# Optimization experiments

Measured on AMD Instinct MI355X. Metric: run time of the kernel, lower is better.

The kernel has to match this reference:

```python
import jax, jax.numpy as jnp
import numpy as np

BN_EPS = 1e-5
TN_EPS = 1e-4


def binarize(x):
    # Clipped straight-through binarization (Courbariaux BNN / Brevitas 1-bit):
    # forward = sign(x) in {-1,+1}, backward = hardtanh STE.
    xc = jnp.clip(x, -1.0, 1.0)
    return xc + jax.lax.stop_gradient(jnp.where(x >= 0, 1.0, -1.0).astype(x.dtype) - xc)


def setup_inputs() -> dict:
    key = jax.random.key(0)
    ks = jax.random.split(key, 20)
    B, D, H, C = 16384, 1024, 1024, 10
    inp = {"x": jax.random.uniform(ks[0], (B, D), dtype=jnp.float32)}
    dims = [(H, D), (H, H), (H, H), (C, H)]
    for i, (o, n) in enumerate(dims):
        inp[f"W{i+1}"] = jax.random.uniform(ks[1 + i], (o, n), minval=-1.0, maxval=1.0, dtype=jnp.float32)
    # BatchNorm1d params (eval mode, running stats) for the 3 hidden layers
    for i in range(3):
        k0, k1, k2, k3 = jax.random.split(ks[5 + i], 4)
        inp[f"g{i+1}"] = 1.0 + 0.1 * jax.random.normal(k0, (H,), dtype=jnp.float32)
        inp[f"b{i+1}"] = 0.1 * jax.random.normal(k1, (H,), dtype=jnp.float32)
        inp[f"m{i+1}"] = 0.1 * jax.random.normal(k2, (H,), dtype=jnp.float32)
        inp[f"v{i+1}"] = 0.5 + jax.random.uniform(k3, (H,), dtype=jnp.float32)
    # TensorNorm (scalar norm on the logits)
    inp["tn_w"] = jnp.ones((), dtype=jnp.float32)
    inp["tn_b"] = jnp.zeros((), dtype=jnp.float32)
    inp["tn_m"] = jnp.zeros((), dtype=jnp.float32)
    inp["tn_v"] = jnp.ones((), dtype=jnp.float32)
    return inp


def reference(x, W1, W2, W3, W4,
              g1, b1, m1, v1,
              g2, b2, m2, v2,
              g3, b3, m3, v3,
              tn_w, tn_b, tn_m, tn_v):
    h = binarize(2.0 * x.reshape(x.shape[0], -1) - 1.0)
    # Dropout is identity in eval mode.
    bn = [(g1, b1, m1, v1), (g2, b2, m2, v2), (g3, b3, m3, v3)]
    for W, (g, b, m, v) in zip((W1, W2, W3), bn):
        h = h @ binarize(W).T                      # [B,H] fake-quant linear, no bias
        h = (h - m) * (g * jax.lax.rsqrt(v + BN_EPS)) + b  # BatchNorm1d eval
        h = binarize(h)                            # 1-bit activation quant
    h = h @ binarize(W4).T                         # [B,10]
    # TensorNorm: scalar affine normalization over the whole tensor
    return (h - tn_m) * jax.lax.rsqrt(tn_v + TN_EPS) * tn_w + tn_b
```

## Files before the change

### kernel.cpp

```cpp
#include <hip/hip_runtime.h>
#include <stdint.h>

typedef int  v4i  __attribute__((ext_vector_type(4)));
typedef int  v16i __attribute__((ext_vector_type(16)));
typedef unsigned int uint32;

#define BATCH 16384
#define FEAT  1024

#define OFF_ACTA 0u
#define OFF_ACTB 16777216u
#define OFF_WA1  33554432u
#define OFF_WA2  34603008u
#define OFF_WA3  35651584u
#define OFF_WA4  36700160u
#define OFF_TH   36732928u

__global__ void __launch_bounds__(256) prep_kernel(
    const float* __restrict__ x,
    const float* __restrict__ W1, const float* __restrict__ W2,
    const float* __restrict__ W3, const float* __restrict__ W4,
    const float* __restrict__ g1, const float* __restrict__ b1,
    const float* __restrict__ m1, const float* __restrict__ v1,
    const float* __restrict__ g2, const float* __restrict__ b2,
    const float* __restrict__ m2, const float* __restrict__ v2,
    const float* __restrict__ g3, const float* __restrict__ b3,
    const float* __restrict__ m3, const float* __restrict__ v3,
    char* __restrict__ actA, char* __restrict__ wa1, char* __restrict__ wa2,
    char* __restrict__ wa3, char* __restrict__ wa4, int2* __restrict__ TH)
{
    int b = blockIdx.x;
    if (b == 609) {
        for (int gid = threadIdx.x; gid < 3072; gid += 256) {
            int l = gid >> 10, j = gid & 1023;
            const float *g, *bb, *m, *v;
            if (l == 0)      { g = g1; bb = b1; m = m1; v = v1; }
            else if (l == 1) { g = g2; bb = b2; m = m2; v = v2; }
            else             { g = g3; bb = b3; m = m3; v = v3; }
            double gd = (double)g[j], bd = (double)bb[j], md = (double)m[j], vd = (double)v[j];
            double s = gd / sqrt(vd + 1e-5);
            int ti, flip;
            if (s > 0.0)      { ti = (int)ceil(md - bd / s);  flip = 0; }
            else if (s < 0.0) { ti = (int)floor(md - bd / s); flip = 1; }
            else              { ti = (bd >= 0.0) ? -2000000 : 2000000; flip = 0; }
            TH[gid] = make_int2(ti, flip);
        }
        return;
    }

    const float* src; char* dst; float thr; int nrows; int dblk;
    if (b < 512)      { src = x  + (size_t)b * 32768;            dst = actA; dblk = b;      thr = 0.5f; nrows = 32; }
    else if (b < 544) { int mb = b - 512; src = W1 + (size_t)mb * 32768; dst = wa1; dblk = mb; thr = 0.0f; nrows = 32; }
    else if (b < 576) { int mb = b - 544; src = W2 + (size_t)mb * 32768; dst = wa2; dblk = mb; thr = 0.0f; nrows = 32; }
    else if (b < 608) { int mb = b - 576; src = W3 + (size_t)mb * 32768; dst = wa3; dblk = mb; thr = 0.0f; nrows = 32; }
    else              { src = W4; dst = wa4; dblk = 0; thr = 0.0f; nrows = 10; }

    __shared__ unsigned char T[32][1040];
#pragma unroll
    for (int u = 0; u < 8; ++u) {
        int unit = threadIdx.x + u * 256;
        int row  = unit >> 6;
        int c16  = (unit & 63) << 4;
        uint32 wb0 = 0, wb1 = 0, wb2 = 0, wb3 = 0;
        if (row < nrows) {
            const float* p = src + (size_t)row * 1024 + c16;
            float4 f0 = *(const float4*)(p + 0);
            float4 f1 = *(const float4*)(p + 4);
            float4 f2 = *(const float4*)(p + 8);
            float4 f3 = *(const float4*)(p + 12);
            wb0 = (f0.x>=thr?0x01u:0xFFu) | ((f0.y>=thr?0x01u:0xFFu)<<8) | ((f0.z>=thr?0x01u:0xFFu)<<16) | ((f0.w>=thr?0x01u:0xFFu)<<24);
            wb1 = (f1.x>=thr?0x01u:0xFFu) | ((f1.y>=thr?0x01u:0xFFu)<<8) | ((f1.z>=thr?0x01u:0xFFu)<<16) | ((f1.w>=thr?0x01u:0xFFu)<<24);
            wb2 = (f2.x>=thr?0x01u:0xFFu) | ((f2.y>=thr?0x01u:0xFFu)<<8) | ((f2.z>=thr?0x01u:0xFFu)<<16) | ((f2.w>=thr?0x01u:0xFFu)<<24);
            wb3 = (f3.x>=thr?0x01u:0xFFu) | ((f3.y>=thr?0x01u:0xFFu)<<8) | ((f3.z>=thr?0x01u:0xFFu)<<16) | ((f3.w>=thr?0x01u:0xFFu)<<24);
        }
        *(uint4*)&T[row][c16] = make_uint4(wb0, wb1, wb2, wb3);
    }
    __syncthreads();

    int lane = threadIdx.x & 63;
    int wv   = threadIdx.x >> 6;
    int row  = lane & 31;
    int hb   = (lane >> 5) * 4;
#pragma unroll
    for (int u = 0; u < 8; ++u) {
        int kk = wv * 8 + u;
        const unsigned char* tr = &T[row][kk * 32 + hb];
        uint32 w0 = *(const uint32*)(tr + 0);
        uint32 w1 = *(const uint32*)(tr + 8);
        uint32 w2 = *(const uint32*)(tr + 16);
        uint32 w3 = *(const uint32*)(tr + 24);
        *(uint4*)(dst + (((size_t)dblk * 32 + kk) * 64 + lane) * 16) = make_uint4(w0, w1, w2, w3);
    }
}

__device__ __forceinline__ void stage_tile(v4i (*Bs)[2048], int bufi,
                                           const v4i* __restrict__ Bin,
                                           int tile, int wv, int lane) {
#pragma unroll
    for (int j = 0; j < 8; ++j) {
        __builtin_amdgcn_global_load_lds(
            (const __attribute__((address_space(1))) void*)
                (Bin + (size_t)tile * 2048 + j * 256 + wv * 64 + lane),
            (__attribute__((address_space(3))) void*)
                (&Bs[bufi][j * 256 + wv * 64]),
            16, 0, 0);
    }
}

__global__ void __launch_bounds__(256, 2) gemm_i8_kernel(
    const v4i* __restrict__ Af, const v4i* __restrict__ Bin,
    const int2* __restrict__ th, v4i* __restrict__ Bout)
{
    __shared__ v4i Bs[2][2048];
    const int tid  = threadIdx.x;
    const int lane = tid & 63;
    const int wv   = tid >> 6;
    int bid = blockIdx.x;
    int xcd = bid & 7;
    int i   = bid >> 3;
    int s   = xcd + ((i >> 3) << 3);
    int m   = i & 7;
    int mt  = m * 4 + wv;
    int nb0 = s * 8;

    stage_tile(Bs, 0, Bin, nb0, wv, lane);

    v4i a[32];
    {
        const v4i* Ap = Af + (size_t)mt * 2048;
#pragma unroll
        for (int kk = 0; kk < 32; ++kk) a[kk] = Ap[kk * 64 + lane];
    }
    int tt[16], tf[16];
    {
        const int2* thp = th + mt * 32;
        int hi4 = (lane >> 5) * 4;
#pragma unroll
        for (int q = 0; q < 16; ++q) {
            int2 t = thp[(q & 3) + 8 * (q >> 2) + hi4];
            tt[q] = t.x; tf[q] = t.y;
        }
    }
    asm volatile("s_waitcnt vmcnt(0)" ::: "memory");
    __builtin_amdgcn_s_barrier();

    int buf = 0;
#pragma unroll 1
    for (int it = 0; it < 8; ++it) {
        if (it < 7) stage_tile(Bs, buf ^ 1, Bin, nb0 + it + 1, wv, lane);

        v16i acc0, acc1;
#pragma unroll
        for (int z = 0; z < 16; ++z) { acc0[z] = 0; acc1[z] = 0; }
#pragma unroll
        for (int kk = 0; kk < 16; ++kk) {
            v4i b0 = Bs[buf][kk * 64 + lane];
            v4i b1 = Bs[buf][(kk + 16) * 64 + lane];
            acc0 = __builtin_amdgcn_mfma_i32_32x32x32_i8(a[kk],      b0, acc0, 0, 0, 0);
            acc1 = __builtin_amdgcn_mfma_i32_32x32x32_i8(a[kk + 16], b1, acc1, 0, 0, 0);
        }

        uint32 wds0 = 0, wds1 = 0, wds2 = 0, wds3 = 0;
#pragma unroll
        for (int bq = 0; bq < 4; ++bq) {
            { int q = bq;      int h = acc0[q] + acc1[q]; int bit = tf[q] ? (h <= tt[q]) : (h >= tt[q]); wds0 |= (bit ? 0x01u : 0xFFu) << (8 * bq); }
            { int q = 4 + bq;  int h = acc0[q] + acc1[q]; int bit = tf[q] ? (h <= tt[q]) : (h >= tt[q]); wds1 |= (bit ? 0x01u : 0xFFu) << (8 * bq); }
            { int q = 8 + bq;  int h = acc0[q] + acc1[q]; int bit = tf[q] ? (h <= tt[q]) : (h >= tt[q]); wds2 |= (bit ? 0x01u : 0xFFu) << (8 * bq); }
            { int q = 12 + bq; int h = acc0[q] + acc1[q]; int bit = tf[q] ? (h <= tt[q]) : (h >= tt[q]); wds3 |= (bit ? 0x01u : 0xFFu) << (8 * bq); }
        }
        v4i ov; ov[0] = (int)wds0; ov[1] = (int)wds1; ov[2] = (int)wds2; ov[3] = (int)wds3;
        Bout[((size_t)(nb0 + it) * 32 + mt) * 64 + lane] = ov;

        if (it < 7) {
            asm volatile("s_waitcnt vmcnt(1)" ::: "memory");
            __builtin_amdgcn_s_barrier();
            buf ^= 1;
        }
    }
}

__global__ void __launch_bounds__(256) final_kernel(
    const v4i* __restrict__ Af4, const v4i* __restrict__ B3,
    const float* __restrict__ tw, const float* __restrict__ tb,
    const float* __restrict__ tm, const float* __restrict__ tv,
    float* __restrict__ out)
{
    int lane = threadIdx.x & 63;
    int nb   = blockIdx.x * 4 + (threadIdx.x >> 6);
    const v4i* Bf = B3 + (size_t)nb * 2048;
    v16i acc;
#pragma unroll
    for (int z = 0; z < 16; ++z) acc[z] = 0;
#pragma unroll
    for (int kk = 0; kk < 32; ++kk) {
        v4i av = Af4[kk * 64 + lane];
        v4i bv = Bf[kk * 64 + lane];
        acc = __builtin_amdgcn_mfma_i32_32x32x32_i8(av, bv, acc, 0, 0, 0);
    }
    double sc  = (double)tw[0] / sqrt((double)tv[0] + 1e-4);
    double off = (double)tb[0] - (double)tm[0] * sc;
    int colg = nb * 32 + (lane & 31);
    int hi   = lane >> 5;
#pragma unroll
    for (int q = 0; q < 8; ++q) {
        int rr = (q & 3) + 8 * (q >> 2) + 4 * hi;
        if (rr < 10)
            out[(size_t)colg * 10 + rr] = (float)((double)acc[q] * sc + off);
    }
}

extern "C" void kernel_launch(void* const* d_in, const int* in_sizes, int n_in,
                              void* d_out, int out_size, void* d_ws, size_t ws_size,
                              hipStream_t stream) {
    const float* x  = (const float*)d_in[0];
    const float* W1 = (const float*)d_in[1];
    const float* W2 = (const float*)d_in[2];
    const float* W3 = (const float*)d_in[3];
    const float* W4 = (const float*)d_in[4];
    const float* g1 = (const float*)d_in[5];
    const float* b1 = (const float*)d_in[6];
    const float* m1 = (const float*)d_in[7];
    const float* v1 = (const float*)d_in[8];
    const float* g2 = (const float*)d_in[9];
    const float* b2 = (const float*)d_in[10];
    const float* m2 = (const float*)d_in[11];
    const float* v2 = (const float*)d_in[12];
    const float* g3 = (const float*)d_in[13];
    const float* b3 = (const float*)d_in[14];
    const float* m3 = (const float*)d_in[15];
    const float* v3 = (const float*)d_in[16];
    const float* tw = (const float*)d_in[17];
    const float* tb = (const float*)d_in[18];
    const float* tm = (const float*)d_in[19];
    const float* tv = (const float*)d_in[20];

    char* ws = (char*)d_ws;
    char* actA = ws + OFF_ACTA;
    char* actB = ws + OFF_ACTB;
    char* wa1  = ws + OFF_WA1;
    char* wa2  = ws + OFF_WA2;
    char* wa3  = ws + OFF_WA3;
    char* wa4  = ws + OFF_WA4;
    int2* TH   = (int2*)(ws + OFF_TH);

    prep_kernel<<<610, 256, 0, stream>>>(x, W1, W2, W3, W4,
                                         g1, b1, m1, v1, g2, b2, m2, v2,
                                         g3, b3, m3, v3,
                                         actA, wa1, wa2, wa3, wa4, TH);

    gemm_i8_kernel<<<512, 256, 0, stream>>>((const v4i*)wa1, (const v4i*)actA, TH,        (v4i*)actB);
    gemm_i8_kernel<<<512, 256, 0, stream>>>((const v4i*)wa2, (const v4i*)actB, TH + 1024, (v4i*)actA);
    gemm_i8_kernel<<<512, 256, 0, stream>>>((const v4i*)wa3, (const v4i*)actA, TH + 2048, (v4i*)actB);

    final_kernel<<<128, 256, 0, stream>>>((const v4i*)wa4, (const v4i*)actB,
                                          tw, tb, tm, tv, (float*)d_out);
}
```

Before: 200.1 us.

## Fold BN sign flip into weights and threshold into accumulator init

Rows of each binarized weight matrix whose BN scale is negative are negated during prep. The threshold then becomes a single int per channel, loaded once into shared memory and preloaded as the negated initial accumulator value. The epilogue reduces to a sign-bit extraction instead of per-element compare and select. The change also double-buffers LDS reads of B fragments in registers ahead of the MFMAs and launches the final kernel as 256 blocks of 128 threads. This trims epilogue ALU work and register pressure from holding threshold arrays, at the cost of a small shared array and per-row gamma reads in prep.

```diff
diff --git a/kernel.cpp b/kernel.cpp
--- a/kernel.cpp
+++ b/kernel.cpp
@@ -27,7 +27,7 @@
     const float* __restrict__ g3, const float* __restrict__ b3,
     const float* __restrict__ m3, const float* __restrict__ v3,
     char* __restrict__ actA, char* __restrict__ wa1, char* __restrict__ wa2,
-    char* __restrict__ wa3, char* __restrict__ wa4, int2* __restrict__ TH)
+    char* __restrict__ wa3, char* __restrict__ wa4, int* __restrict__ TH)
 {
     int b = blockIdx.x;
     if (b == 609) {
@@ -39,20 +39,21 @@
             else             { g = g3; bb = b3; m = m3; v = v3; }
             double gd = (double)g[j], bd = (double)bb[j], md = (double)m[j], vd = (double)v[j];
             double s = gd / sqrt(vd + 1e-5);
-            int ti, flip;
-            if (s > 0.0)      { ti = (int)ceil(md - bd / s);  flip = 0; }
-            else if (s < 0.0) { ti = (int)floor(md - bd / s); flip = 1; }
-            else              { ti = (bd >= 0.0) ? -2000000 : 2000000; flip = 0; }
-            TH[gid] = make_int2(ti, flip);
+            int t2;
+            if (s > 0.0)      t2 = (int)ceil(md - bd / s);
+            else if (s < 0.0) t2 = -(int)floor(md - bd / s);
+            else              t2 = (bd >= 0.0) ? -2000000 : 2000000;
+            TH[gid] = t2;
         }
         return;
     }
 
     const float* src; char* dst; float thr; int nrows; int dblk;
+    const float* gp = nullptr;
     if (b < 512)      { src = x  + (size_t)b * 32768;            dst = actA; dblk = b;      thr = 0.5f; nrows = 32; }
-    else if (b < 544) { int mb = b - 512; src = W1 + (size_t)mb * 32768; dst = wa1; dblk = mb; thr = 0.0f; nrows = 32; }
-    else if (b < 576) { int mb = b - 544; src = W2 + (size_t)mb * 32768; dst = wa2; dblk = mb; thr = 0.0f; nrows = 32; }
-    else if (b < 608) { int mb = b - 576; src = W3 + (size_t)mb * 32768; dst = wa3; dblk = mb; thr = 0.0f; nrows = 32; }
+    else if (b < 544) { int mb = b - 512; src = W1 + (size_t)mb * 32768; dst = wa1; dblk = mb; thr = 0.0f; nrows = 32; gp = g1; }
+    else if (b < 576) { int mb = b - 544; src = W2 + (size_t)mb * 32768; dst = wa2; dblk = mb; thr = 0.0f; nrows = 32; gp = g2; }
+    else if (b < 608) { int mb = b - 576; src = W3 + (size_t)mb * 32768; dst = wa3; dblk = mb; thr = 0.0f; nrows = 32; gp = g3; }
     else              { src = W4; dst = wa4; dblk = 0; thr = 0.0f; nrows = 10; }
 
     __shared__ unsigned char T[32][1040];
@@ -63,15 +64,18 @@
         int c16  = (unit & 63) << 4;
         uint32 wb0 = 0, wb1 = 0, wb2 = 0, wb3 = 0;
         if (row < nrows) {
+            bool flipb = gp && (gp[dblk * 32 + row] < 0.0f);
             const float* p = src + (size_t)row * 1024 + c16;
             float4 f0 = *(const float4*)(p + 0);
             float4 f1 = *(const float4*)(p + 4);
             float4 f2 = *(const float4*)(p + 8);
             float4 f3 = *(const float4*)(p + 12);
-            wb0 = (f0.x>=thr?0x01u:0xFFu) | ((f0.y>=thr?0x01u:0xFFu)<<8) | ((f0.z>=thr?0x01u:0xFFu)<<16) | ((f0.w>=thr?0x01u:0xFFu)<<24);
-            wb1 = (f1.x>=thr?0x01u:0xFFu) | ((f1.y>=thr?0x01u:0xFFu)<<8) | ((f1.z>=thr?0x01u:0xFFu)<<16) | ((f1.w>=thr?0x01u:0xFFu)<<24);
-            wb2 = (f2.x>=thr?0x01u:0xFFu) | ((f2.y>=thr?0x01u:0xFFu)<<8) | ((f2.z>=thr?0x01u:0xFFu)<<16) | ((f2.w>=thr?0x01u:0xFFu)<<24);
-            wb3 = (f3.x>=thr?0x01u:0xFFu) | ((f3.y>=thr?0x01u:0xFFu)<<8) | ((f3.z>=thr?0x01u:0xFFu)<<16) | ((f3.w>=thr?0x01u:0xFFu)<<24);
+#define BY(f) ((((f) >= thr) != flipb) ? 0x01u : 0xFFu)
+            wb0 = BY(f0.x) | (BY(f0.y)<<8) | (BY(f0.z)<<16) | (BY(f0.w)<<24);
+            wb1 = BY(f1.x) | (BY(f1.y)<<8) | (BY(f1.z)<<16) | (BY(f1.w)<<24);
+            wb2 = BY(f2.x) | (BY(f2.y)<<8) | (BY(f2.z)<<16) | (BY(f2.w)<<24);
+            wb3 = BY(f3.x) | (BY(f3.y)<<8) | (BY(f3.z)<<16) | (BY(f3.w)<<24);
+#undef BY
         }
         *(uint4*)&T[row][c16] = make_uint4(wb0, wb1, wb2, wb3);
     }
@@ -109,9 +113,10 @@
 
 __global__ void __launch_bounds__(256, 2) gemm_i8_kernel(
     const v4i* __restrict__ Af, const v4i* __restrict__ Bin,
-    const int2* __restrict__ th, v4i* __restrict__ Bout)
+    const int* __restrict__ th, v4i* __restrict__ Bout)
 {
     __shared__ v4i Bs[2][2048];
+    __shared__ int Tsh[128];
     const int tid  = threadIdx.x;
     const int lane = tid & 63;
     const int wv   = tid >> 6;
@@ -124,6 +129,7 @@
     int nb0 = s * 8;
 
     stage_tile(Bs, 0, Bin, nb0, wv, lane);
+    if (tid < 128) Tsh[tid] = th[m * 128 + tid];
 
     v4i a[32];
     {
@@ -131,19 +137,10 @@
 #pragma unroll
         for (int kk = 0; kk < 32; ++kk) a[kk] = Ap[kk * 64 + lane];
     }
-    int tt[16], tf[16];
-    {
-        const int2* thp = th + mt * 32;
-        int hi4 = (lane >> 5) * 4;
-#pragma unroll
-        for (int q = 0; q < 16; ++q) {
-            int2 t = thp[(q & 3) + 8 * (q >> 2) + hi4];
-            tt[q] = t.x; tf[q] = t.y;
-        }
-    }
-    asm volatile("s_waitcnt vmcnt(0)" ::: "memory");
+    asm volatile("s_waitcnt vmcnt(0) lgkmcnt(0)" ::: "memory");
     __builtin_amdgcn_s_barrier();
 
+    const int hi4 = (lane >> 5) * 4;
     int buf = 0;
 #pragma unroll 1
     for (int it = 0; it < 8; ++it) {
@@ -151,22 +148,32 @@
 
         v16i acc0, acc1;
 #pragma unroll
-        for (int z = 0; z < 16; ++z) { acc0[z] = 0; acc1[z] = 0; }
+        for (int q = 0; q < 16; ++q) {
+            acc0[q] = -Tsh[wv * 32 + (q & 3) + 8 * (q >> 2) + hi4];
+            acc1[q] = 0;
+        }
+
+        v4i b0 = Bs[buf][lane];
+        v4i b1 = Bs[buf][16 * 64 + lane];
 #pragma unroll
         for (int kk = 0; kk < 16; ++kk) {
-            v4i b0 = Bs[buf][kk * 64 + lane];
-            v4i b1 = Bs[buf][(kk + 16) * 64 + lane];
+            v4i nb0f, nb1f;
+            if (kk < 15) {
+                nb0f = Bs[buf][(kk + 1) * 64 + lane];
+                nb1f = Bs[buf][(kk + 17) * 64 + lane];
+            }
             acc0 = __builtin_amdgcn_mfma_i32_32x32x32_i8(a[kk],      b0, acc0, 0, 0, 0);
             acc1 = __builtin_amdgcn_mfma_i32_32x32x32_i8(a[kk + 16], b1, acc1, 0, 0, 0);
+            b0 = nb0f; b1 = nb1f;
         }
 
         uint32 wds0 = 0, wds1 = 0, wds2 = 0, wds3 = 0;
 #pragma unroll
         for (int bq = 0; bq < 4; ++bq) {
-            { int q = bq;      int h = acc0[q] + acc1[q]; int bit = tf[q] ? (h <= tt[q]) : (h >= tt[q]); wds0 |= (bit ? 0x01u : 0xFFu) << (8 * bq); }
-            { int q = 4 + bq;  int h = acc0[q] + acc1[q]; int bit = tf[q] ? (h <= tt[q]) : (h >= tt[q]); wds1 |= (bit ? 0x01u : 0xFFu) << (8 * bq); }
-            { int q = 8 + bq;  int h = acc0[q] + acc1[q]; int bit = tf[q] ? (h <= tt[q]) : (h >= tt[q]); wds2 |= (bit ? 0x01u : 0xFFu) << (8 * bq); }
-            { int q = 12 + bq; int h = acc0[q] + acc1[q]; int bit = tf[q] ? (h <= tt[q]) : (h >= tt[q]); wds3 |= (bit ? 0x01u : 0xFFu) << (8 * bq); }
+            { int h = acc0[bq]      + acc1[bq];      wds0 |= (((uint32)((h >> 31) | 1)) & 0xFFu) << (8 * bq); }
+            { int h = acc0[4 + bq]  + acc1[4 + bq];  wds1 |= (((uint32)((h >> 31) | 1)) & 0xFFu) << (8 * bq); }
+            { int h = acc0[8 + bq]  + acc1[8 + bq];  wds2 |= (((uint32)((h >> 31) | 1)) & 0xFFu) << (8 * bq); }
+            { int h = acc0[12 + bq] + acc1[12 + bq]; wds3 |= (((uint32)((h >> 31) | 1)) & 0xFFu) << (8 * bq); }
         }
         v4i ov; ov[0] = (int)wds0; ov[1] = (int)wds1; ov[2] = (int)wds2; ov[3] = (int)wds3;
         Bout[((size_t)(nb0 + it) * 32 + mt) * 64 + lane] = ov;
@@ -179,14 +186,14 @@
     }
 }
 
-__global__ void __launch_bounds__(256) final_kernel(
+__global__ void __launch_bounds__(128) final_kernel(
     const v4i* __restrict__ Af4, const v4i* __restrict__ B3,
     const float* __restrict__ tw, const float* __restrict__ tb,
     const float* __restrict__ tm, const float* __restrict__ tv,
     float* __restrict__ out)
 {
     int lane = threadIdx.x & 63;
-    int nb   = blockIdx.x * 4 + (threadIdx.x >> 6);
+    int nb   = blockIdx.x * 2 + (threadIdx.x >> 6);
     const v4i* Bf = B3 + (size_t)nb * 2048;
     v16i acc;
 #pragma unroll
@@ -241,7 +248,7 @@
     char* wa2  = ws + OFF_WA2;
     char* wa3  = ws + OFF_WA3;
     char* wa4  = ws + OFF_WA4;
-    int2* TH   = (int2*)(ws + OFF_TH);
+    int*  TH   = (int*)(ws + OFF_TH);
 
     prep_kernel<<<610, 256, 0, stream>>>(x, W1, W2, W3, W4,
                                          g1, b1, m1, v1, g2, b2, m2, v2,
@@ -252,6 +259,6 @@
     gemm_i8_kernel<<<512, 256, 0, stream>>>((const v4i*)wa2, (const v4i*)actB, TH + 1024, (v4i*)actA);
     gemm_i8_kernel<<<512, 256, 0, stream>>>((const v4i*)wa3, (const v4i*)actA, TH + 2048, (v4i*)actB);
 
-    final_kernel<<<128, 256, 0, stream>>>((const v4i*)wa4, (const v4i*)actB,
+    final_kernel<<<256, 128, 0, stream>>>((const v4i*)wa4, (const v4i*)actB,
                                           tw, tb, tm, tv, (float*)d_out);
 }
```

After: 202.9 us. Within noise of the previous version (+1.4%).
